# Kernel tuning notes

Measured on AMD Instinct MI355X. Metric: run time of the kernel, lower is better.

The kernel has to match this reference:

```python
import jax, jax.numpy as jnp
import numpy as np
import math

C_IN = 256
INTER = 64  # max(256//4, 8)
MAX_SIZE = 64
TEMP = 1.0


def setup_inputs() -> dict:
    key = jax.random.key(0)
    ks = jax.random.split(key, 12)
    B, C, H, W = 16, C_IN, 64, 64
    x = jax.random.normal(ks[0], (B, C, H, W), dtype=jnp.float32)
    pos_embedding = jax.random.normal(ks[1], (1, INTER, MAX_SIZE, MAX_SIZE), dtype=jnp.float32) * 0.02
    # 1x1 conv weights stored as [out, in] (kernel spatial dims are 1)
    def xavier(k, out_c, in_c):
        bound = math.sqrt(6.0 / (in_c + out_c))
        return jax.random.uniform(k, (out_c, in_c), dtype=jnp.float32, minval=-bound, maxval=bound)
    wq = xavier(ks[2], INTER, C)
    wk = xavier(ks[3], INTER, C)
    wv = xavier(ks[4], INTER, C)
    wo = xavier(ks[5], C, INTER)
    bq = jnp.zeros((INTER,), jnp.float32)
    bk = jnp.zeros((INTER,), jnp.float32)
    bv = jnp.zeros((INTER,), jnp.float32)
    bo = jnp.zeros((C,), jnp.float32)
    gamma = jnp.ones((1,), jnp.float32) * 0.1
    return {"x": x, "pos_embedding": pos_embedding, "wq": wq, "bq": bq,
            "wk": wk, "bk": bk, "wv": wv, "bv": bv, "wo": wo, "bo": bo,
            "gamma": gamma}


def reference(x, pos_embedding, wq, bq, wk, bk, wv, bv, wo, bo, gamma):
    B, C, H, W = x.shape
    N = H * W
    pos = pos_embedding[:, :, :H, :W]  # [1, INTER, H, W]

    def conv1x1(w, b, inp):
        # [out,in] x [B,in,H,W] -> [B,out,H,W]
        return jnp.einsum('oc,bchw->bohw', w, inp) + b[None, :, None, None]

    q = conv1x1(wq, bq, x) + pos
    k = conv1x1(wk, bk, x) + pos
    v = conv1x1(wv, bv, x)

    # flatten spatial -> tokens: [B, N, INTER]
    q = q.reshape(B, INTER, N).transpose(0, 2, 1)
    k = k.reshape(B, INTER, N).transpose(0, 2, 1)
    v = v.reshape(B, INTER, N).transpose(0, 2, 1)

    scale = 1.0 / (TEMP * math.sqrt(INTER))
    logits = jnp.einsum('bnd,bmd->bnm', q, k) * scale  # [B, N, N]
    attn = jax.nn.softmax(logits, axis=-1)
    attended = jnp.einsum('bnm,bmd->bnd', attn, v)  # [B, N, INTER]

    attended = attended.transpose(0, 2, 1).reshape(B, INTER, H, W)
    out = conv1x1(wo, bo, attended)
    return gamma * out + x
```

## Files before the change

### kernel.cpp

```cpp
#include <hip/hip_runtime.h>

typedef unsigned short u16;
typedef unsigned int u32;
typedef __attribute__((ext_vector_type(8))) short short8;
typedef __attribute__((ext_vector_type(4))) float f32x4;

#define DEV static __device__ __forceinline__

DEV u16 f2bf(float f) {
  u32 u = __builtin_bit_cast(u32, f);
  u += 0x7FFFu + ((u >> 16) & 1u);
  return (u16)(u >> 16);
}
DEV u32 cvtpk(float a, float b) {
  u32 d;
  asm("v_cvt_pk_bf16_f32 %0, %1, %2" : "=v"(d) : "v"(a), "v"(b));
  return d;
}
DEV short8 ld8(const u16* p) {
  uint4 v = *reinterpret_cast<const uint4*>(p);
  return __builtin_bit_cast(short8, v);
}

#define BB 16
#define CC 256
#define DD 64
#define NN 4096

__global__ __launch_bounds__(256) void prep_kernel(
    const float* __restrict__ wq, const float* __restrict__ wk,
    const float* __restrict__ wv, const float* __restrict__ wo,
    u16* __restrict__ wqb, u16* __restrict__ wkb,
    u16* __restrict__ wvb, u16* __restrict__ wob)
{
  int i = blockIdx.x * 256 + threadIdx.x;
  wqb[i] = f2bf(wq[i]);
  wkb[i] = f2bf(wk[i]);
  wvb[i] = f2bf(wv[i]);
  wob[i] = f2bf(wo[i]);
}

__global__ __launch_bounds__(256, 4) void qkv_kernel(
    const float* __restrict__ xg, const float* __restrict__ pos_e,
    const u16* __restrict__ wqb, const u16* __restrict__ wkb,
    const u16* __restrict__ wvb,
    const float* __restrict__ bq, const float* __restrict__ bk,
    const float* __restrict__ bv,
    u16* __restrict__ Qb, u16* __restrict__ Kb, u16* __restrict__ Vt)
{
  const int nc = blockIdx.x, b = blockIdx.y, tid = threadIdx.x;
  const int n0 = nc * 64;
  __shared__ u16 Xs[64 * 256];

  {
    const int ng = tid & 15;
    const int ch0 = tid >> 4;
#pragma unroll
    for (int it = 0; it < 2; ++it) {
      const int c0 = (ch0 + 16 * it) * 8;
      f32x4 xv[8];
#pragma unroll
      for (int j = 0; j < 8; ++j)
        xv[j] = *reinterpret_cast<const f32x4*>(
            xg + ((size_t)(b * CC + c0 + j)) * NN + n0 + ng * 4);
#pragma unroll
      for (int i = 0; i < 4; ++i) {
        const int n = ng * 4 + i;
        uint4 o;
        o.x = cvtpk(xv[0][i], xv[1][i]);
        o.y = cvtpk(xv[2][i], xv[3][i]);
        o.z = cvtpk(xv[4][i], xv[5][i]);
        o.w = cvtpk(xv[6][i], xv[7][i]);
        *reinterpret_cast<uint4*>(&Xs[n * 256 + (c0 ^ ((n & 7) * 8))]) = o;
      }
    }
  }
  __syncthreads();

  const int w = tid >> 6, lane = tid & 63, lc = lane & 15, quad = lane >> 4;
  const int swz = (lc & 7) * 8;

  const u16* wsp[3];
  int gsel[3];
#pragma unroll
  for (int j = 0; j < 3; ++j) {
    const int nt = w * 3 + j;
    wsp[j] = (nt < 4) ? wqb : (nt < 8) ? wkb : wvb;
    gsel[j] = nt & 3;
  }

  f32x4 acc[3][4];
#pragma unroll
  for (int j = 0; j < 3; ++j)
#pragma unroll
    for (int ns = 0; ns < 4; ++ns) acc[j][ns] = (f32x4){0.f, 0.f, 0.f, 0.f};

#pragma unroll
  for (int kk = 0; kk < 8; ++kk) {
    short8 bf[3], af[4];
#pragma unroll
    for (int j = 0; j < 3; ++j)
      bf[j] = ld8(wsp[j] + (size_t)(gsel[j] * 16 + lc) * CC + kk * 32 + quad * 8);
#pragma unroll
    for (int ns = 0; ns < 4; ++ns)
      af[ns] = ld8(&Xs[(ns * 16 + lc) * 256 + ((kk * 32 + quad * 8) ^ swz)]);
#pragma unroll
    for (int j = 0; j < 3; ++j)
#pragma unroll
      for (int ns = 0; ns < 4; ++ns)
        acc[j][ns] = __builtin_amdgcn_mfma_f32_16x16x32_bf16(af[ns], bf[j], acc[j][ns], 0, 0, 0);
  }

  f32x4 posv[3][4];
#pragma unroll
  for (int j = 0; j < 3; ++j) {
    const int nt = w * 3 + j;
    if (nt < 8) {
#pragma unroll
      for (int ns = 0; ns < 4; ++ns)
        posv[j][ns] = *reinterpret_cast<const f32x4*>(
            pos_e + (size_t)(gsel[j] * 16 + lc) * NN + n0 + ns * 16 + quad * 4);
    }
  }

  __syncthreads();
  u16* Vst = Xs;

#pragma unroll
  for (int j = 0; j < 3; ++j) {
    const int nt = w * 3 + j;
    const int ch = gsel[j] * 16 + lc;
    const float bias = (nt < 4) ? bq[ch] : (nt < 8) ? bk[ch] : bv[ch];
#pragma unroll
    for (int ns = 0; ns < 4; ++ns) {
      if (nt < 8) {
        u16* dst = (nt < 4) ? Qb : Kb;
#pragma unroll
        for (int r = 0; r < 4; ++r) {
          const int n = n0 + ns * 16 + quad * 4 + r;
          float v = acc[j][ns][r] + bias;
          v += posv[j][ns][r];
          if (nt < 4) v *= 0.125f;
          dst[((size_t)(b * NN + n)) * DD + ch] = f2bf(v);
        }
      } else {
        uint2 o2;
        o2.x = cvtpk(acc[j][ns][0] + bias, acc[j][ns][1] + bias);
        o2.y = cvtpk(acc[j][ns][2] + bias, acc[j][ns][3] + bias);
        *reinterpret_cast<uint2*>(
            &Vst[ch * 64 + ((ns * 16 + quad * 4) ^ ((ch & 7) * 8))]) = o2;
      }
    }
  }
  __syncthreads();

  {
    const int ch = tid >> 2, part = tid & 3;
    const int sw = (ch & 7) * 8;
    const uint4 a  = *reinterpret_cast<const uint4*>(&Vst[ch * 64 + ((part * 16) ^ sw)]);
    const uint4 c2 = *reinterpret_cast<const uint4*>(&Vst[ch * 64 + ((part * 16 + 8) ^ sw)]);
    u16* dst = Vt + ((size_t)(b * DD + ch)) * NN + n0 + part * 16;
    *reinterpret_cast<uint4*>(dst) = a;
    *reinterpret_cast<uint4*>(dst + 8) = c2;
  }
}

#define QB 128

__global__ __launch_bounds__(512, 4) void flash_kernel(
    const u16* __restrict__ Qg, const u16* __restrict__ Kg,
    const u16* __restrict__ Vtg,
    const u16* __restrict__ wob, const float* __restrict__ bo,
    const float* __restrict__ gam, const float* __restrict__ xg,
    float* __restrict__ outg)
{
  const int qt = blockIdx.x, b = blockIdx.y, tid = threadIdx.x;
  const int w = tid >> 6, lane = tid & 63, lc = lane & 15, quad = lane >> 4;
  const int swz = (lc & 7) * 8;
  __shared__ u16 Ks[2][64 * 64];
  __shared__ u16 Vs[2][64 * 64];
  __shared__ u16 Ps[8][16 * 64];

  const u16* Kbase = Kg + (size_t)b * NN * DD;
  const u16* Vbase = Vtg + (size_t)b * DD * NN;

  const int r = tid >> 3, seg = (tid & 7) * 8;
  const int sdst = r * 64 + (seg ^ ((r & 7) * 8));
  const u16* kp = Kbase + (size_t)r * DD + seg;
  const u16* vp = Vbase + (size_t)r * NN + seg;

  const int qrow = qt * QB + w * 16 + lc;
  short8 qf[2];
#pragma unroll
  for (int kk = 0; kk < 2; ++kk)
    qf[kk] = ld8(Qg + ((size_t)(b * NN + qrow)) * DD + kk * 32 + quad * 8);

  uint4 kr = *reinterpret_cast<const uint4*>(kp);
  uint4 vr = *reinterpret_cast<const uint4*>(vp);
  *reinterpret_cast<uint4*>(&Ks[0][sdst]) = kr;
  *reinterpret_cast<uint4*>(&Vs[0][sdst]) = vr;
  __syncthreads();

  f32x4 O[4];
#pragma unroll
  for (int i = 0; i < 4; ++i) O[i] = (f32x4){0.f, 0.f, 0.f, 0.f};
  float lsum = 0.f;

  for (int kt = 0; kt < 64; ++kt) {
    const int cur = kt & 1;
    if (kt < 63) {
      kr = *reinterpret_cast<const uint4*>(kp + (size_t)(kt + 1) * (64 * DD));
      vr = *reinterpret_cast<const uint4*>(vp + (kt + 1) * 64);
    }

    f32x4 S[4];
#pragma unroll
    for (int mf = 0; mf < 4; ++mf) {
      S[mf] = (f32x4){0.f, 0.f, 0.f, 0.f};
#pragma unroll
      for (int kk = 0; kk < 2; ++kk) {
        short8 af = ld8(&Ks[cur][(mf * 16 + lc) * 64 + ((kk * 32 + quad * 8) ^ swz)]);
        S[mf] = __builtin_amdgcn_mfma_f32_16x16x32_bf16(af, qf[kk], S[mf], 0, 0, 0);
      }
    }

    float p[16];
#pragma unroll
    for (int mf = 0; mf < 4; ++mf)
#pragma unroll
      for (int i = 0; i < 4; ++i) {
        float e = __expf(fminf(S[mf][i], 80.f));
        p[mf * 4 + i] = e;
        lsum += e;
      }

#pragma unroll
    for (int mf = 0; mf < 4; ++mf) {
      uint2 pkk;
      pkk.x = cvtpk(p[mf * 4 + 0], p[mf * 4 + 1]);
      pkk.y = cvtpk(p[mf * 4 + 2], p[mf * 4 + 3]);
      *reinterpret_cast<uint2*>(&Ps[w][lc * 64 + ((mf * 16 + quad * 4) ^ swz)]) = pkk;
    }
    short8 pf[2];
#pragma unroll
    for (int kk = 0; kk < 2; ++kk)
      pf[kk] = ld8(&Ps[w][lc * 64 + ((kk * 32 + quad * 8) ^ swz)]);

#pragma unroll
    for (int dmf = 0; dmf < 4; ++dmf)
#pragma unroll
      for (int kk = 0; kk < 2; ++kk) {
        short8 vf = ld8(&Vs[cur][(dmf * 16 + lc) * 64 + ((kk * 32 + quad * 8) ^ swz)]);
        O[dmf] = __builtin_amdgcn_mfma_f32_16x16x32_bf16(vf, pf[kk], O[dmf], 0, 0, 0);
      }

    if (kt < 63) {
      const int nxt = cur ^ 1;
      *reinterpret_cast<uint4*>(&Ks[nxt][sdst]) = kr;
      *reinterpret_cast<uint4*>(&Vs[nxt][sdst]) = vr;
      __syncthreads();
    }
  }

  lsum += __shfl_xor(lsum, 16);
  lsum += __shfl_xor(lsum, 32);
  const float rl = 1.0f / lsum;

  u16* AttS = &Ps[0][0];
#pragma unroll
  for (int mf = 0; mf < 4; ++mf) {
    uint2 o2;
    o2.x = cvtpk(O[mf][0] * rl, O[mf][1] * rl);
    o2.y = cvtpk(O[mf][2] * rl, O[mf][3] * rl);
    *reinterpret_cast<uint2*>(
        &AttS[(w * 16 + lc) * 64 + ((mf * 16 + quad * 4) ^ swz)]) = o2;
  }
  __syncthreads();

  f32x4 acc[2][8];
#pragma unroll
  for (int i = 0; i < 2; ++i)
#pragma unroll
    for (int j = 0; j < 8; ++j) acc[i][j] = (f32x4){0.f, 0.f, 0.f, 0.f};

#pragma unroll
  for (int kk = 0; kk < 2; ++kk) {
    short8 bfr[8];
#pragma unroll
    for (int nt = 0; nt < 8; ++nt)
      bfr[nt] = ld8(&AttS[(nt * 16 + lc) * 64 + ((kk * 32 + quad * 8) ^ swz)]);
#pragma unroll
    for (int mti = 0; mti < 2; ++mti) {
      short8 af = ld8(wob + (size_t)(w * 32 + mti * 16 + lc) * DD + kk * 32 + quad * 8);
#pragma unroll
      for (int nt = 0; nt < 8; ++nt)
        acc[mti][nt] = __builtin_amdgcn_mfma_f32_16x16x32_bf16(af, bfr[nt], acc[mti][nt], 0, 0, 0);
    }
  }

  const float g = gam[0];
  const int n0 = qt * QB;
#pragma unroll
  for (int mti = 0; mti < 2; ++mti)
#pragma unroll
    for (int rr = 0; rr < 4; ++rr) {
      const int co = w * 32 + mti * 16 + quad * 4 + rr;
      const float bov = bo[co];
#pragma unroll
      for (int nt = 0; nt < 8; ++nt) {
        const int n = n0 + nt * 16 + lc;
        const size_t idx = ((size_t)(b * CC + co)) * NN + n;
        outg[idx] = g * (acc[mti][nt][rr] + bov) + xg[idx];
      }
    }
}

extern "C" void kernel_launch(void* const* d_in, const int* in_sizes, int n_in,
                              void* d_out, int out_size, void* d_ws, size_t ws_size,
                              hipStream_t stream) {
  const float* x   = (const float*)d_in[0];
  const float* pos = (const float*)d_in[1];
  const float* wq  = (const float*)d_in[2];
  const float* bq  = (const float*)d_in[3];
  const float* wk  = (const float*)d_in[4];
  const float* bk  = (const float*)d_in[5];
  const float* wv  = (const float*)d_in[6];
  const float* bv  = (const float*)d_in[7];
  const float* wo  = (const float*)d_in[8];
  const float* bo  = (const float*)d_in[9];
  const float* gm  = (const float*)d_in[10];
  float* out = (float*)d_out;

  u16* Qb  = (u16*)d_ws;
  u16* Kb  = Qb + (size_t)BB * NN * DD;
  u16* Vt  = Kb + (size_t)BB * NN * DD;
  u16* wqb = Vt + (size_t)BB * NN * DD;
  u16* wkb = wqb + 16384;
  u16* wvb = wkb + 16384;
  u16* wob = wvb + 16384;

  dim3 blk(256);
  prep_kernel<<<dim3(64), blk, 0, stream>>>(wq, wk, wv, wo, wqb, wkb, wvb, wob);
  qkv_kernel<<<dim3(64, 16), blk, 0, stream>>>(x, pos, wqb, wkb, wvb, bq, bk, bv, Qb, Kb, Vt);
  flash_kernel<<<dim3(32, 16), dim3(512), 0, stream>>>(Qb, Kb, Vt, wob, bo, gm, x, out);
}
```

Before: 250.2 us.

## Use 32x32 MFMA with register-resident P and split-K key halves across waves

Replaces the 16x16x32 MFMA flash loop with 32x32x16 MFMAs. Each group of four waves owns 32 query rows and each half of the block processes half of every 64-key tile. The P fragments are built in registers with v_permlane32_swap, so the per-wave LDS round-trip for P goes away. Partial O and row-sum results from the two key halves are reduced through shared memory before the output projection. This is meant to cut LDS traffic and MFMA instruction count in the inner loop, at the cost of an extra cross-wave reduction, larger accumulator register use, and s_setprio hints.

```diff
diff --git a/kernel.cpp b/kernel.cpp
--- a/kernel.cpp
+++ b/kernel.cpp
@@ -4,6 +4,7 @@
 typedef unsigned int u32;
 typedef __attribute__((ext_vector_type(8))) short short8;
 typedef __attribute__((ext_vector_type(4))) float f32x4;
+typedef __attribute__((ext_vector_type(16))) float f32x16;
 
 #define DEV static __device__ __forceinline__
 
@@ -20,6 +21,18 @@
 DEV short8 ld8(const u16* p) {
   uint4 v = *reinterpret_cast<const uint4*>(p);
   return __builtin_bit_cast(short8, v);
+}
+
+DEV short8 frag8(const float* p) {
+  u32 a0 = cvtpk(p[0], p[1]);
+  u32 a1 = cvtpk(p[2], p[3]);
+  u32 b0 = cvtpk(p[4], p[5]);
+  u32 b1 = cvtpk(p[6], p[7]);
+  asm("v_permlane32_swap_b32 %0, %1" : "+v"(a0), "+v"(b0));
+  asm("v_permlane32_swap_b32 %0, %1" : "+v"(a1), "+v"(b1));
+  uint4 u;
+  u.x = a0; u.y = a1; u.z = b0; u.w = b1;
+  return __builtin_bit_cast(short8, u);
 }
 
 #define BB 16
@@ -175,35 +188,40 @@
     float* __restrict__ outg)
 {
   const int qt = blockIdx.x, b = blockIdx.y, tid = threadIdx.x;
-  const int w = tid >> 6, lane = tid & 63, lc = lane & 15, quad = lane >> 4;
-  const int swz = (lc & 7) * 8;
-  __shared__ u16 Ks[2][64 * 64];
-  __shared__ u16 Vs[2][64 * 64];
-  __shared__ u16 Ps[8][16 * 64];
+  const int w = tid >> 6, lane = tid & 63;
+  const int l31 = lane & 31, hi8 = (lane >> 5) * 8;
+  const int swz = (l31 & 7) * 8;
+  const int khalf = w >> 2;
+  const int qg = w & 3;
+
+  __shared__ u16 pool[25088];
+  u16* const KsA = pool;
+  u16* const VsA = pool + 8192;
+  u16* const AttS = pool + 16384;
+  float* const poolF = reinterpret_cast<float*>(pool);
 
   const u16* Kbase = Kg + (size_t)b * NN * DD;
   const u16* Vbase = Vtg + (size_t)b * DD * NN;
 
-  const int r = tid >> 3, seg = (tid & 7) * 8;
-  const int sdst = r * 64 + (seg ^ ((r & 7) * 8));
-  const u16* kp = Kbase + (size_t)r * DD + seg;
-  const u16* vp = Vbase + (size_t)r * NN + seg;
-
-  const int qrow = qt * QB + w * 16 + lc;
-  short8 qf[2];
-#pragma unroll
-  for (int kk = 0; kk < 2; ++kk)
-    qf[kk] = ld8(Qg + ((size_t)(b * NN + qrow)) * DD + kk * 32 + quad * 8);
+  const int sr = tid >> 3, seg = (tid & 7) * 8;
+  const int sdst = sr * 64 + (seg ^ ((sr & 7) * 8));
+  const u16* kp = Kbase + (size_t)sr * DD + seg;
+  const u16* vp = Vbase + (size_t)sr * NN + seg;
+
+  const int qrow = qt * QB + qg * 32 + l31;
+  short8 qf[4];
+#pragma unroll
+  for (int kk = 0; kk < 4; ++kk)
+    qf[kk] = ld8(Qg + ((size_t)(b * NN + qrow)) * DD + kk * 16 + hi8);
 
   uint4 kr = *reinterpret_cast<const uint4*>(kp);
   uint4 vr = *reinterpret_cast<const uint4*>(vp);
-  *reinterpret_cast<uint4*>(&Ks[0][sdst]) = kr;
-  *reinterpret_cast<uint4*>(&Vs[0][sdst]) = vr;
-  __syncthreads();
-
-  f32x4 O[4];
-#pragma unroll
-  for (int i = 0; i < 4; ++i) O[i] = (f32x4){0.f, 0.f, 0.f, 0.f};
+  *reinterpret_cast<uint4*>(&KsA[sdst]) = kr;
+  *reinterpret_cast<uint4*>(&VsA[sdst]) = vr;
+  __syncthreads();
+
+  f32x16 O0 = (f32x16)0.0f;
+  f32x16 O1 = (f32x16)0.0f;
   float lsum = 0.f;
 
   for (int kt = 0; kt < 64; ++kt) {
@@ -212,71 +230,104 @@
       kr = *reinterpret_cast<const uint4*>(kp + (size_t)(kt + 1) * (64 * DD));
       vr = *reinterpret_cast<const uint4*>(vp + (kt + 1) * 64);
     }
-
-    f32x4 S[4];
-#pragma unroll
-    for (int mf = 0; mf < 4; ++mf) {
-      S[mf] = (f32x4){0.f, 0.f, 0.f, 0.f};
-#pragma unroll
-      for (int kk = 0; kk < 2; ++kk) {
-        short8 af = ld8(&Ks[cur][(mf * 16 + lc) * 64 + ((kk * 32 + quad * 8) ^ swz)]);
-        S[mf] = __builtin_amdgcn_mfma_f32_16x16x32_bf16(af, qf[kk], S[mf], 0, 0, 0);
-      }
-    }
+    const u16* Kc = KsA + cur * 4096;
+    const u16* Vc = VsA + cur * 4096;
+
+    f32x16 S = (f32x16)0.0f;
+    __builtin_amdgcn_s_setprio(1);
+#pragma unroll
+    for (int kk = 0; kk < 4; ++kk) {
+      short8 af = ld8(&Kc[(khalf * 32 + l31) * 64 + ((kk * 16 + hi8) ^ swz)]);
+      S = __builtin_amdgcn_mfma_f32_32x32x16_bf16(af, qf[kk], S, 0, 0, 0);
+    }
+    __builtin_amdgcn_s_setprio(0);
 
     float p[16];
 #pragma unroll
-    for (int mf = 0; mf < 4; ++mf)
-#pragma unroll
-      for (int i = 0; i < 4; ++i) {
-        float e = __expf(fminf(S[mf][i], 80.f));
-        p[mf * 4 + i] = e;
-        lsum += e;
-      }
-
-#pragma unroll
-    for (int mf = 0; mf < 4; ++mf) {
-      uint2 pkk;
-      pkk.x = cvtpk(p[mf * 4 + 0], p[mf * 4 + 1]);
-      pkk.y = cvtpk(p[mf * 4 + 2], p[mf * 4 + 3]);
-      *reinterpret_cast<uint2*>(&Ps[w][lc * 64 + ((mf * 16 + quad * 4) ^ swz)]) = pkk;
-    }
-    short8 pf[2];
-#pragma unroll
-    for (int kk = 0; kk < 2; ++kk)
-      pf[kk] = ld8(&Ps[w][lc * 64 + ((kk * 32 + quad * 8) ^ swz)]);
-
-#pragma unroll
-    for (int dmf = 0; dmf < 4; ++dmf)
-#pragma unroll
-      for (int kk = 0; kk < 2; ++kk) {
-        short8 vf = ld8(&Vs[cur][(dmf * 16 + lc) * 64 + ((kk * 32 + quad * 8) ^ swz)]);
-        O[dmf] = __builtin_amdgcn_mfma_f32_16x16x32_bf16(vf, pf[kk], O[dmf], 0, 0, 0);
-      }
+    for (int r = 0; r < 16; ++r) {
+      float e = __expf(fminf(S[r], 80.f));
+      p[r] = e;
+      lsum += e;
+    }
+
+    short8 pf0 = frag8(&p[0]);
+    short8 pf1 = frag8(&p[8]);
+
+    __builtin_amdgcn_s_setprio(1);
+#pragma unroll
+    for (int kf = 0; kf < 2; ++kf) {
+      const short8 pfv = kf ? pf1 : pf0;
+      const int ko = (khalf * 32 + kf * 16 + hi8) ^ swz;
+      short8 v0 = ld8(&Vc[l31 * 64 + ko]);
+      O0 = __builtin_amdgcn_mfma_f32_32x32x16_bf16(v0, pfv, O0, 0, 0, 0);
+      short8 v1 = ld8(&Vc[(32 + l31) * 64 + ko]);
+      O1 = __builtin_amdgcn_mfma_f32_32x32x16_bf16(v1, pfv, O1, 0, 0, 0);
+    }
+    __builtin_amdgcn_s_setprio(0);
 
     if (kt < 63) {
       const int nxt = cur ^ 1;
-      *reinterpret_cast<uint4*>(&Ks[nxt][sdst]) = kr;
-      *reinterpret_cast<uint4*>(&Vs[nxt][sdst]) = vr;
+      *reinterpret_cast<uint4*>(&KsA[nxt * 4096 + sdst]) = kr;
+      *reinterpret_cast<uint4*>(&VsA[nxt * 4096 + sdst]) = vr;
       __syncthreads();
     }
   }
 
-  lsum += __shfl_xor(lsum, 16);
+  __syncthreads();
+
   lsum += __shfl_xor(lsum, 32);
-  const float rl = 1.0f / lsum;
-
-  u16* AttS = &Ps[0][0];
-#pragma unroll
-  for (int mf = 0; mf < 4; ++mf) {
-    uint2 o2;
-    o2.x = cvtpk(O[mf][0] * rl, O[mf][1] * rl);
-    o2.y = cvtpk(O[mf][2] * rl, O[mf][3] * rl);
-    *reinterpret_cast<uint2*>(
-        &AttS[(w * 16 + lc) * 64 + ((mf * 16 + quad * 4) ^ swz)]) = o2;
-  }
-  __syncthreads();
-
+
+  if (w >= 4) {
+    const int base = ((w - 4) * 64 + lane) * 32;
+#pragma unroll
+    for (int i = 0; i < 4; ++i) {
+      f32x4 t0 = {O0[i * 4 + 0], O0[i * 4 + 1], O0[i * 4 + 2], O0[i * 4 + 3]};
+      *reinterpret_cast<f32x4*>(&poolF[base + ((i * 4) ^ ((lane & 7) * 4))]) = t0;
+      f32x4 t1 = {O1[i * 4 + 0], O1[i * 4 + 1], O1[i * 4 + 2], O1[i * 4 + 3]};
+      *reinterpret_cast<f32x4*>(&poolF[base + ((16 + i * 4) ^ ((lane & 7) * 4))]) = t1;
+    }
+    poolF[12288 + (w - 4) * 64 + lane] = lsum;
+  }
+  __syncthreads();
+
+  if (w < 4) {
+    const int base = (w * 64 + lane) * 32;
+#pragma unroll
+    for (int i = 0; i < 4; ++i) {
+      f32x4 t0 = *reinterpret_cast<const f32x4*>(&poolF[base + ((i * 4) ^ ((lane & 7) * 4))]);
+      f32x4 t1 = *reinterpret_cast<const f32x4*>(&poolF[base + ((16 + i * 4) ^ ((lane & 7) * 4))]);
+#pragma unroll
+      for (int j = 0; j < 4; ++j) {
+        O0[i * 4 + j] += t0[j];
+        O1[i * 4 + j] += t1[j];
+      }
+    }
+    lsum += poolF[12288 + w * 64 + lane];
+    const float rl = 1.0f / lsum;
+
+    const int nl = w * 32 + l31;
+    float a[16];
+#pragma unroll
+    for (int r = 0; r < 16; ++r) a[r] = O0[r] * rl;
+    short8 f0 = frag8(&a[0]);
+    short8 f1 = frag8(&a[8]);
+    *reinterpret_cast<uint4*>(&AttS[nl * 64 + ((0 + hi8) ^ swz)]) =
+        __builtin_bit_cast(uint4, f0);
+    *reinterpret_cast<uint4*>(&AttS[nl * 64 + ((16 + hi8) ^ swz)]) =
+        __builtin_bit_cast(uint4, f1);
+#pragma unroll
+    for (int r = 0; r < 16; ++r) a[r] = O1[r] * rl;
+    f0 = frag8(&a[0]);
+    f1 = frag8(&a[8]);
+    *reinterpret_cast<uint4*>(&AttS[nl * 64 + ((32 + hi8) ^ swz)]) =
+        __builtin_bit_cast(uint4, f0);
+    *reinterpret_cast<uint4*>(&AttS[nl * 64 + ((48 + hi8) ^ swz)]) =
+        __builtin_bit_cast(uint4, f1);
+  }
+  __syncthreads();
+
+  const int lc = lane & 15, quad = lane >> 4;
+  const int swz16 = (lc & 7) * 8;
   f32x4 acc[2][8];
 #pragma unroll
   for (int i = 0; i < 2; ++i)
@@ -288,7 +339,7 @@
     short8 bfr[8];
 #pragma unroll
     for (int nt = 0; nt < 8; ++nt)
-      bfr[nt] = ld8(&AttS[(nt * 16 + lc) * 64 + ((kk * 32 + quad * 8) ^ swz)]);
+      bfr[nt] = ld8(&AttS[(nt * 16 + lc) * 64 + ((kk * 32 + quad * 8) ^ swz16)]);
 #pragma unroll
     for (int mti = 0; mti < 2; ++mti) {
       short8 af = ld8(wob + (size_t)(w * 32 + mti * 16 + lc) * DD + kk * 32 + quad * 8);
```

New measurement: 249.8 us. Within noise of the previous version (-0.2%).
